# Kernel tuning notes

Hardware: AMD Instinct MI355X
Metric: run time of the kernel (lower is better)

## Reference

```python
import jax, jax.numpy as jnp
import numpy as np

IMG_SIZE = 512
NUM_FREQ_MASKS = 4


def _make_masks(n, num):
    # Mirrors DCTTransform._generate_freq_masks: for i in reversed(range(num-1)),
    # an anti-triangular (low-frequency) mask of size n//2**i padded to (n,n),
    # then an all-ones mask appended last.
    masks = []
    for i in reversed(range(num - 1)):
        m = n // (2 ** i)
        tri = np.triu(np.ones((m, m), dtype=np.float32))      # upper triangular
        rot = np.rot90(tri, k=1)                               # -> i+j <= m-1 region
        pad = np.zeros((n, n), dtype=np.float32)
        pad[:m, :m] = rot
        masks.append(pad)
    masks.append(np.ones((n, n), dtype=np.float32))
    return np.stack(masks)  # [num, n, n]


def _dct_matrix(n, dtype=jnp.float32):
    # Orthonormal DCT-II matrix: X = D @ x  ==  scipy.fftpack.dct(x, axis=0, norm='ortho')
    k = jnp.arange(n, dtype=dtype)[:, None]
    m = jnp.arange(n, dtype=dtype)[None, :]
    D = jnp.cos(jnp.pi * (2.0 * m + 1.0) * k / (2.0 * n)) * jnp.sqrt(2.0 / n)
    D = D.at[0].multiply(1.0 / jnp.sqrt(2.0))  # k=0 row scale -> sqrt(1/n)
    return D


def setup_inputs() -> dict:
    key = jax.random.key(0)
    x = jax.random.normal(key, (32, 3, IMG_SIZE, IMG_SIZE), dtype=jnp.float32)
    masks = jnp.asarray(_make_masks(IMG_SIZE, NUM_FREQ_MASKS))
    return {"x": x, "masks": masks}


def reference(x, masks):
    # x: [B, C, H, W] with H == W == img_size; masks: [4, H, W]
    n = x.shape[-1]
    D = _dct_matrix(n, x.dtype)
    # 2D orthonormal DCT-II over last two axes: D @ x @ D^T (separable, order-free)
    dct2 = jnp.einsum('ij,bcjk,lk->bcil', D, x, D)
    outs = []
    for i in range(masks.shape[0]):  # small fixed loop over 4 masks
        masked = dct2 * masks[i]
        # inverse 2D DCT (IDCT-II == DCT-III, orthonormal): D^T @ y @ D
        outs.append(jnp.einsum('ji,bcjk,kl->bcil', D, masked, D))
    LH, HL, HH, LL = outs  # idx 0->LH, 1->HL, 2->HH, 3(ones)->LL per original forward
    return (LL, LH, HL, HH)
```

## Files before the change

### kernel.cpp

```cpp
#include <hip/hip_runtime.h>
#include <hip/hip_bf16.h>
#include <stdint.h>

#define NIMG 96
#define N 512
#define IMG (N*N)
#define OUT_PLANE ((long long)NIMG * IMG)

typedef __attribute__((ext_vector_type(8))) _Float16 f16x8;
typedef __attribute__((ext_vector_type(4))) float f32x4;
typedef unsigned short u16;

__device__ inline u16 f2h(float v) {
    _Float16 h = (_Float16)v;
    return __builtin_bit_cast(u16, h);
}

__device__ inline void gload16(const void* g, void* l) {
    __builtin_amdgcn_global_load_lds(
        (const __attribute__((address_space(1))) void*)g,
        (__attribute__((address_space(3))) void*)l, 16, 0, 0);
}

__global__ void build_D(u16* __restrict__ Drm, u16* __restrict__ Dcm) {
    int idx = blockIdx.x * 256 + threadIdx.x;
    int k = idx >> 9, m = idx & 511;
    int r = ((2 * m + 1) * k) & 2047;
    float c = cospif((float)r * (1.0f / 1024.0f));
    float s = (k == 0) ? 0.04419417382415922f : 0.0625f;
    u16 h = f2h(c * s);
    Drm[k * 512 + m] = h;
    Dcm[m * 512 + k] = h;
}

__global__ __launch_bounds__(256) void conv_x(const float* __restrict__ x,
                                              u16* __restrict__ Xcm) {
    __shared__ float t[32][33];
    const long long base = (long long)blockIdx.z * IMG;
    const int r0 = blockIdx.y * 32, c0 = blockIdx.x * 32;
    const int tr = threadIdx.x >> 3;
    const int tc = (threadIdx.x & 7) * 4;
    float4 v = *(const float4*)&x[base + (long long)(r0 + tr) * N + c0 + tc];
    t[tr][tc + 0] = v.x; t[tr][tc + 1] = v.y;
    t[tr][tc + 2] = v.z; t[tr][tc + 3] = v.w;
    __syncthreads();
    ushort4 h;
    h.x = f2h(t[tc + 0][tr]); h.y = f2h(t[tc + 1][tr]);
    h.z = f2h(t[tc + 2][tr]); h.w = f2h(t[tc + 3][tr]);
    *(ushort4*)&Xcm[base + (long long)(c0 + tr) * N + r0 + tc] = h;
}

__global__ __launch_bounds__(256) void maskcopy(const u16* __restrict__ Y,
                                                u16* __restrict__ Z,
                                                int W, int lim) {
    long long idx = (long long)blockIdx.x * 256 + threadIdx.x;
    int wq = W >> 2;
    long long perimg = (long long)W * wq;
    int img = (int)(idx / perimg);
    long long rem = idx % perimg;
    int j = (int)(rem / wq);
    int i = (int)(rem % wq) * 4;
    ushort4 v = *(const ushort4*)&Y[(long long)img * IMG + (long long)j * N + i];
    if (i + 0 + j > lim) v.x = 0;
    if (i + 1 + j > lim) v.y = 0;
    if (i + 2 + j > lim) v.z = 0;
    if (i + 3 + j > lim) v.w = 0;
    *(ushort4*)&Z[(long long)img * W * W + (long long)j * W + i] = v;
}

template<int EPI>
__global__ __launch_bounds__(256) void gemm16(
    const u16* __restrict__ A, long long sA, int lda,
    const u16* __restrict__ B, long long sB, int ldb,
    void* __restrict__ Cv, long long sC, int ldc,
    int K, int trilim)
{
    __shared__ u16 As[2][128 * 32];
    __shared__ u16 Bs[2][128 * 32];

    const int bz = blockIdx.z;
    const int m0 = blockIdx.y * 128;
    const int n0 = blockIdx.x * 128;
    const int tid = threadIdx.x;
    const int wave = tid >> 6;
    const int lane = tid & 63;

    const u16* __restrict__ Ab = A + (long long)bz * sA;
    const u16* __restrict__ Bb = B + (long long)bz * sB;

    const int srow = lane >> 2;
    const int sc8  = (lane & 3) * 8;
    const int war  = wave * 32;

    const int fr  = lane & 15;
    const int kg8 = (lane >> 4) * 8;
    const int wr  = (wave >> 1) * 64;
    const int wc  = (wave & 1) * 64;

    int aoff[4], boff[4];
    #pragma unroll
    for (int i = 0; i < 4; ++i) {
        aoff[i] = (wr + i * 16 + fr) * 32 + kg8;
        boff[i] = (wc + i * 16 + fr) * 32 + kg8;
    }

    f32x4 acc[4][4];
    #pragma unroll
    for (int i = 0; i < 4; ++i)
        #pragma unroll
        for (int j = 0; j < 4; ++j)
            acc[i][j] = (f32x4){0.0f, 0.0f, 0.0f, 0.0f};

    auto stage = [&](int buf, int k0) {
        #pragma unroll
        for (int i = 0; i < 2; ++i) {
            int r = war + i * 16;
            gload16(Ab + (long long)(m0 + r + srow) * lda + k0 + sc8, &As[buf][r * 32]);
            gload16(Bb + (long long)(n0 + r + srow) * ldb + k0 + sc8, &Bs[buf][r * 32]);
        }
    };
    auto compute = [&](int buf) {
        f16x8 af[4], bf[4];
        #pragma unroll
        for (int i = 0; i < 4; ++i) af[i] = *(const f16x8*)&As[buf][aoff[i]];
        #pragma unroll
        for (int j = 0; j < 4; ++j) bf[j] = *(const f16x8*)&Bs[buf][boff[j]];
        #pragma unroll
        for (int i = 0; i < 4; ++i)
            #pragma unroll
            for (int j = 0; j < 4; ++j)
                acc[i][j] = __builtin_amdgcn_mfma_f32_16x16x32_f16(af[i], bf[j], acc[i][j], 0, 0, 0);
    };

    const int nb = K >> 5;
    stage(0, 0);
    __syncthreads();
    int cur = 0;
    for (int t = 0; t < nb - 1; ++t) {
        stage(cur ^ 1, (t + 1) * 32);
        compute(cur);
        __syncthreads();
        cur ^= 1;
    }
    compute(cur);

    const int rb = (lane >> 4) * 4;
    if (EPI == 0) {
        float* Cb = (float*)Cv + (long long)bz * sC;
        #pragma unroll
        for (int i = 0; i < 4; ++i)
            #pragma unroll
            for (int j = 0; j < 4; ++j) {
                int r = m0 + wr + i * 16 + rb;
                int c = n0 + wc + j * 16 + fr;
                #pragma unroll
                for (int g = 0; g < 4; ++g)
                    Cb[(long long)(r + g) * ldc + c] = acc[i][j][g];
            }
    } else if (EPI == 1) {
        u16* Cb = (u16*)Cv + (long long)bz * sC;
        #pragma unroll
        for (int i = 0; i < 4; ++i)
            #pragma unroll
            for (int j = 0; j < 4; ++j) {
                int r = m0 + wr + i * 16 + rb;
                int c = n0 + wc + j * 16 + fr;
                #pragma unroll
                for (int g = 0; g < 4; ++g)
                    Cb[(long long)(r + g) * ldc + c] = f2h(acc[i][j][g]);
            }
    } else {
        u16* Cb = (u16*)Cv + (long long)bz * sC;
        #pragma unroll
        for (int i = 0; i < 4; ++i)
            #pragma unroll
            for (int j = 0; j < 4; ++j) {
                int r = m0 + wr + i * 16 + rb;
                int c = n0 + wc + j * 16 + fr;
                ushort4 h;
                float v0 = ((r + 0) + c <= trilim) ? acc[i][j][0] : 0.0f;
                float v1 = ((r + 1) + c <= trilim) ? acc[i][j][1] : 0.0f;
                float v2 = ((r + 2) + c <= trilim) ? acc[i][j][2] : 0.0f;
                float v3 = ((r + 3) + c <= trilim) ? acc[i][j][3] : 0.0f;
                h.x = f2h(v0); h.y = f2h(v1); h.z = f2h(v2); h.w = f2h(v3);
                *(ushort4*)&Cb[(long long)c * ldc + r] = h;
            }
    }
}

extern "C" void kernel_launch(void* const* d_in, const int* in_sizes, int n_in,
                              void* d_out, int out_size, void* d_ws, size_t ws_size,
                              hipStream_t stream) {
    const float* x = (const float*)d_in[0];
    float* out = (float*)d_out;
    float* outLL = out + 0 * OUT_PLANE;
    float* outLH = out + 1 * OUT_PLANE;
    float* outHL = out + 2 * OUT_PLANE;
    float* outHH = out + 3 * OUT_PLANE;

    char* ws = (char*)d_ws;
    u16* Drm = (u16*)(ws);
    u16* Dcm = (u16*)(ws + 524288);
    u16* Xcm = (u16*)(ws + 1048576);
    u16* Ycm = Xcm;
    char* reg = ws + 51380224;
    u16* T1 = (u16*)reg;
    u16* U  = (u16*)reg;
    u16* U2 = (u16*)reg;
    u16* U3 = (u16*)reg;
    u16* Y2 = (u16*)(reg + 25165824);
    u16* Y3 = (u16*)(reg + 37748736);

    const long long S = IMG;
    const int BIG = 1 << 30;

    build_D<<<dim3(IMG / 256), 256, 0, stream>>>(Drm, Dcm);
    conv_x<<<dim3(16, 16, NIMG), 256, 0, stream>>>(x, Xcm);

    gemm16<1><<<dim3(4, 4, NIMG), 256, 0, stream>>>(
        Drm, 0, 512, Xcm, S, 512, T1, S, 512, 512, 0);
    gemm16<2><<<dim3(4, 4, NIMG), 256, 0, stream>>>(
        T1, S, 512, Drm, 0, 512, Ycm, S, 512, 512, 511);
    gemm16<2><<<dim3(4, 4, NIMG), 256, 0, stream>>>(
        Ycm, S, 512, Dcm, 0, 512, U, S, 512, 512, BIG);
    gemm16<0><<<dim3(4, 4, NIMG), 256, 0, stream>>>(
        U, S, 512, Dcm, 0, 512, outHH, S, 512, 512, 0);

    maskcopy<<<dim3(NIMG * 256 * 256 / 4 / 256), 256, 0, stream>>>(Ycm, Y2, 256, 255);
    maskcopy<<<dim3(NIMG * 128 * 128 / 4 / 256), 256, 0, stream>>>(Ycm, Y3, 128, 127);

    gemm16<2><<<dim3(4, 2, NIMG), 256, 0, stream>>>(
        Y2, 256 * 256, 256, Dcm, 0, 512, U2, 512 * 256, 256, 256, BIG);
    gemm16<0><<<dim3(4, 4, NIMG), 256, 0, stream>>>(
        U2, 512 * 256, 256, Dcm, 0, 512, outHL, S, 512, 256, 0);

    gemm16<2><<<dim3(4, 1, NIMG), 256, 0, stream>>>(
        Y3, 128 * 128, 128, Dcm, 0, 512, U3, 512 * 128, 128, 128, BIG);
    gemm16<0><<<dim3(4, 4, NIMG), 256, 0, stream>>>(
        U3, 512 * 128, 128, Dcm, 0, 512, outLH, S, 512, 128, 0);

    hipMemcpyAsync(outLL, x, (size_t)OUT_PLANE * sizeof(float),
                   hipMemcpyDeviceToDevice, stream);
}
```

Before: 364.0 us.

## Fuse LL copy and mask copies into producers, and skip zero triangular work

The LL output copy now happens inside conv_x, which already reads x, so the separate device-to-device memcpy goes away. The two maskcopy kernels are removed: a new EPI==3 epilogue writes the masked 256×256 and 128×128 coefficient blocks directly, staged in the outLH buffer before that buffer is overwritten. The GEMMs also use the triangular sparsity of the masked spectrum. Tiles entirely above the anti-diagonal skip their MFMA loop and just write zeros, and a kcap parameter shortens the K loop for the inverse-DCT GEMM on the triangular input. The changes are meant to cut redundant global memory traffic, kernel launches and zero FLOPs, at the cost of more epilogue branching and reusing an output buffer as scratch.

Result: no change. 366.4 us (+0.7%).

```diff
diff --git a/kernel.cpp b/kernel.cpp
--- a/kernel.cpp
+++ b/kernel.cpp
@@ -34,13 +34,15 @@
 }
 
 __global__ __launch_bounds__(256) void conv_x(const float* __restrict__ x,
-                                              u16* __restrict__ Xcm) {
+                                              u16* __restrict__ Xcm,
+                                              float* __restrict__ outLL) {
     __shared__ float t[32][33];
     const long long base = (long long)blockIdx.z * IMG;
     const int r0 = blockIdx.y * 32, c0 = blockIdx.x * 32;
     const int tr = threadIdx.x >> 3;
     const int tc = (threadIdx.x & 7) * 4;
     float4 v = *(const float4*)&x[base + (long long)(r0 + tr) * N + c0 + tc];
+    *(float4*)&outLL[base + (long long)(r0 + tr) * N + c0 + tc] = v;
     t[tr][tc + 0] = v.x; t[tr][tc + 1] = v.y;
     t[tr][tc + 2] = v.z; t[tr][tc + 3] = v.w;
     __syncthreads();
@@ -50,30 +52,13 @@
     *(ushort4*)&Xcm[base + (long long)(c0 + tr) * N + r0 + tc] = h;
 }
 
-__global__ __launch_bounds__(256) void maskcopy(const u16* __restrict__ Y,
-                                                u16* __restrict__ Z,
-                                                int W, int lim) {
-    long long idx = (long long)blockIdx.x * 256 + threadIdx.x;
-    int wq = W >> 2;
-    long long perimg = (long long)W * wq;
-    int img = (int)(idx / perimg);
-    long long rem = idx % perimg;
-    int j = (int)(rem / wq);
-    int i = (int)(rem % wq) * 4;
-    ushort4 v = *(const ushort4*)&Y[(long long)img * IMG + (long long)j * N + i];
-    if (i + 0 + j > lim) v.x = 0;
-    if (i + 1 + j > lim) v.y = 0;
-    if (i + 2 + j > lim) v.z = 0;
-    if (i + 3 + j > lim) v.w = 0;
-    *(ushort4*)&Z[(long long)img * W * W + (long long)j * W + i] = v;
-}
-
 template<int EPI>
 __global__ __launch_bounds__(256) void gemm16(
     const u16* __restrict__ A, long long sA, int lda,
     const u16* __restrict__ B, long long sB, int ldb,
     void* __restrict__ Cv, long long sC, int ldc,
-    int K, int trilim)
+    int K, int trilim, int kcap,
+    u16* __restrict__ Y2, u16* __restrict__ Y3)
 {
     __shared__ u16 As[2][128 * 32];
     __shared__ u16 Bs[2][128 * 32];
@@ -111,38 +96,43 @@
         for (int j = 0; j < 4; ++j)
             acc[i][j] = (f32x4){0.0f, 0.0f, 0.0f, 0.0f};
 
-    auto stage = [&](int buf, int k0) {
-        #pragma unroll
-        for (int i = 0; i < 2; ++i) {
-            int r = war + i * 16;
-            gload16(Ab + (long long)(m0 + r + srow) * lda + k0 + sc8, &As[buf][r * 32]);
-            gload16(Bb + (long long)(n0 + r + srow) * ldb + k0 + sc8, &Bs[buf][r * 32]);
+    const bool skip = (EPI == 3) && (m0 + n0 > trilim);
+    const int Keff = (kcap - m0 < K) ? (kcap - m0) : K;
+
+    if (!skip) {
+        auto stage = [&](int buf, int k0) {
+            #pragma unroll
+            for (int i = 0; i < 2; ++i) {
+                int r = war + i * 16;
+                gload16(Ab + (long long)(m0 + r + srow) * lda + k0 + sc8, &As[buf][r * 32]);
+                gload16(Bb + (long long)(n0 + r + srow) * ldb + k0 + sc8, &Bs[buf][r * 32]);
+            }
+        };
+        auto compute = [&](int buf) {
+            f16x8 af[4], bf[4];
+            #pragma unroll
+            for (int i = 0; i < 4; ++i) af[i] = *(const f16x8*)&As[buf][aoff[i]];
+            #pragma unroll
+            for (int j = 0; j < 4; ++j) bf[j] = *(const f16x8*)&Bs[buf][boff[j]];
+            #pragma unroll
+            for (int i = 0; i < 4; ++i)
+                #pragma unroll
+                for (int j = 0; j < 4; ++j)
+                    acc[i][j] = __builtin_amdgcn_mfma_f32_16x16x32_f16(af[i], bf[j], acc[i][j], 0, 0, 0);
+        };
+
+        const int nb = Keff >> 5;
+        stage(0, 0);
+        __syncthreads();
+        int cur = 0;
+        for (int t = 0; t < nb - 1; ++t) {
+            stage(cur ^ 1, (t + 1) * 32);
+            compute(cur);
+            __syncthreads();
+            cur ^= 1;
         }
-    };
-    auto compute = [&](int buf) {
-        f16x8 af[4], bf[4];
-        #pragma unroll
-        for (int i = 0; i < 4; ++i) af[i] = *(const f16x8*)&As[buf][aoff[i]];
-        #pragma unroll
-        for (int j = 0; j < 4; ++j) bf[j] = *(const f16x8*)&Bs[buf][boff[j]];
-        #pragma unroll
-        for (int i = 0; i < 4; ++i)
-            #pragma unroll
-            for (int j = 0; j < 4; ++j)
-                acc[i][j] = __builtin_amdgcn_mfma_f32_16x16x32_f16(af[i], bf[j], acc[i][j], 0, 0, 0);
-    };
-
-    const int nb = K >> 5;
-    stage(0, 0);
-    __syncthreads();
-    int cur = 0;
-    for (int t = 0; t < nb - 1; ++t) {
-        stage(cur ^ 1, (t + 1) * 32);
         compute(cur);
-        __syncthreads();
-        cur ^= 1;
     }
-    compute(cur);
 
     const int rb = (lane >> 4) * 4;
     if (EPI == 0) {
@@ -171,19 +161,39 @@
             }
     } else {
         u16* Cb = (u16*)Cv + (long long)bz * sC;
+        u16* Y2b = (EPI == 3) ? Y2 + (long long)bz * (256 * 256) : nullptr;
+        u16* Y3b = (EPI == 3) ? Y3 + (long long)bz * (128 * 128) : nullptr;
         #pragma unroll
         for (int i = 0; i < 4; ++i)
             #pragma unroll
             for (int j = 0; j < 4; ++j) {
                 int r = m0 + wr + i * 16 + rb;
                 int c = n0 + wc + j * 16 + fr;
-                ushort4 h;
                 float v0 = ((r + 0) + c <= trilim) ? acc[i][j][0] : 0.0f;
                 float v1 = ((r + 1) + c <= trilim) ? acc[i][j][1] : 0.0f;
                 float v2 = ((r + 2) + c <= trilim) ? acc[i][j][2] : 0.0f;
                 float v3 = ((r + 3) + c <= trilim) ? acc[i][j][3] : 0.0f;
+                ushort4 h;
                 h.x = f2h(v0); h.y = f2h(v1); h.z = f2h(v2); h.w = f2h(v3);
                 *(ushort4*)&Cb[(long long)c * ldc + r] = h;
+                if (EPI == 3) {
+                    if (r < 256 && c < 256) {
+                        ushort4 h2;
+                        h2.x = ((r + 0) + c <= 255) ? h.x : (u16)0;
+                        h2.y = ((r + 1) + c <= 255) ? h.y : (u16)0;
+                        h2.z = ((r + 2) + c <= 255) ? h.z : (u16)0;
+                        h2.w = ((r + 3) + c <= 255) ? h.w : (u16)0;
+                        *(ushort4*)&Y2b[(long long)c * 256 + r] = h2;
+                    }
+                    if (r < 128 && c < 128) {
+                        ushort4 h3;
+                        h3.x = ((r + 0) + c <= 127) ? h.x : (u16)0;
+                        h3.y = ((r + 1) + c <= 127) ? h.y : (u16)0;
+                        h3.z = ((r + 2) + c <= 127) ? h.z : (u16)0;
+                        h3.w = ((r + 3) + c <= 127) ? h.w : (u16)0;
+                        *(ushort4*)&Y3b[(long long)c * 128 + r] = h3;
+                    }
+                }
             }
     }
 }
@@ -208,37 +218,31 @@
     u16* U  = (u16*)reg;
     u16* U2 = (u16*)reg;
     u16* U3 = (u16*)reg;
-    u16* Y2 = (u16*)(reg + 25165824);
-    u16* Y3 = (u16*)(reg + 37748736);
+    u16* Y2 = (u16*)outLH;
+    u16* Y3 = (u16*)outLH + (long long)NIMG * 256 * 256;
 
     const long long S = IMG;
     const int BIG = 1 << 30;
 
     build_D<<<dim3(IMG / 256), 256, 0, stream>>>(Drm, Dcm);
-    conv_x<<<dim3(16, 16, NIMG), 256, 0, stream>>>(x, Xcm);
+    conv_x<<<dim3(16, 16, NIMG), 256, 0, stream>>>(x, Xcm, outLL);
 
     gemm16<1><<<dim3(4, 4, NIMG), 256, 0, stream>>>(
-        Drm, 0, 512, Xcm, S, 512, T1, S, 512, 512, 0);
+        Drm, 0, 512, Xcm, S, 512, T1, S, 512, 512, 0, BIG, nullptr, nullptr);
+    gemm16<3><<<dim3(4, 4, NIMG), 256, 0, stream>>>(
+        T1, S, 512, Drm, 0, 512, Ycm, S, 512, 512, 511, BIG, Y2, Y3);
     gemm16<2><<<dim3(4, 4, NIMG), 256, 0, stream>>>(
-        T1, S, 512, Drm, 0, 512, Ycm, S, 512, 512, 511);
-    gemm16<2><<<dim3(4, 4, NIMG), 256, 0, stream>>>(
-        Ycm, S, 512, Dcm, 0, 512, U, S, 512, 512, BIG);
+        Ycm, S, 512, Dcm, 0, 512, U, S, 512, 512, BIG, 512, nullptr, nullptr);
     gemm16<0><<<dim3(4, 4, NIMG), 256, 0, stream>>>(
-        U, S, 512, Dcm, 0, 512, outHH, S, 512, 512, 0);
-
-    maskcopy<<<dim3(NIMG * 256 * 256 / 4 / 256), 256, 0, stream>>>(Ycm, Y2, 256, 255);
-    maskcopy<<<dim3(NIMG * 128 * 128 / 4 / 256), 256, 0, stream>>>(Ycm, Y3, 128, 127);
+        U, S, 512, Dcm, 0, 512, outHH, S, 512, 512, 0, BIG, nullptr, nullptr);
 
     gemm16<2><<<dim3(4, 2, NIMG), 256, 0, stream>>>(
-        Y2, 256 * 256, 256, Dcm, 0, 512, U2, 512 * 256, 256, 256, BIG);
+        Y2, 256 * 256, 256, Dcm, 0, 512, U2, 512 * 256, 256, 256, BIG, 256, nullptr, nullptr);
     gemm16<0><<<dim3(4, 4, NIMG), 256, 0, stream>>>(
-        U2, 512 * 256, 256, Dcm, 0, 512, outHL, S, 512, 256, 0);
+        U2, 512 * 256, 256, Dcm, 0, 512, outHL, S, 512, 256, 0, BIG, nullptr, nullptr);
 
     gemm16<2><<<dim3(4, 1, NIMG), 256, 0, stream>>>(
-        Y3, 128 * 128, 128, Dcm, 0, 512, U3, 512 * 128, 128, 128, BIG);
+        Y3, 128 * 128, 128, Dcm, 0, 512, U3, 512 * 128, 128, 128, BIG, BIG, nullptr, nullptr);
     gemm16<0><<<dim3(4, 4, NIMG), 256, 0, stream>>>(
-        U3, 512 * 128, 128, Dcm, 0, 512, outLH, S, 512, 128, 0);
-
-    hipMemcpyAsync(outLL, x, (size_t)OUT_PLANE * sizeof(float),
-                   hipMemcpyDeviceToDevice, stream);
-}
+        U3, 512 * 128, 128, Dcm, 0, 512, outLH, S, 512, 128, 0, BIG, nullptr, nullptr);
+}
```
